# Kernel optimization log

Hardware: AMD Instinct MI355X
Metric: run time of the kernel (lower is better)

## Reference

```python
import jax, jax.numpy as jnp
import numpy as np

N = 100000
E = 3200000
IN_DIM, HID, RED, EMB = 2, 64, 32, 32
LN_EPS = 1e-5


def gcn_conv(x, W, b, row, col, w_full, dinv):
    # x:[N,F_in] W:[F_in,F_out]; PyG GCNConv: lin (no bias) -> normalized scatter-add -> + bias
    xw = x @ W                                  # [N,F_out]
    norm = dinv[row] * w_full * dinv[col]       # [E+N]
    msgs = norm[:, None] * xw[row]              # gather from source nodes
    out = jax.ops.segment_sum(msgs, col, num_segments=N)
    return out + b


def layer_norm(x, g, b):
    mu = jnp.mean(x, axis=-1, keepdims=True)
    var = jnp.mean((x - mu) ** 2, axis=-1, keepdims=True)
    return (x - mu) * jax.lax.rsqrt(var + LN_EPS) * g + b


def setup_inputs() -> dict:
    key = jax.random.key(0)
    ks = jax.random.split(key, 12)
    def glorot(k, shape):
        lim = float(np.sqrt(6.0 / (shape[0] + shape[1])))
        return jax.random.uniform(k, shape, jnp.float32, -lim, lim)
    return {
        "x": jax.random.normal(ks[0], (N, IN_DIM), jnp.float32),
        "edge_weight": jax.random.uniform(ks[1], (E,), jnp.float32),
        "W1": glorot(ks[2], (IN_DIM, HID)), "b1": jnp.zeros((HID,), jnp.float32),
        "rW1": glorot(ks[3], (IN_DIM, HID)), "rb1": jnp.zeros((HID,), jnp.float32),
        "g1": jnp.ones((HID,), jnp.float32), "be1": jnp.zeros((HID,), jnp.float32),
        "W2": glorot(ks[4], (HID, RED)), "b2": jnp.zeros((RED,), jnp.float32),
        "rW2": glorot(ks[5], (HID, RED)), "rb2": jnp.zeros((RED,), jnp.float32),
        "g2": jnp.ones((RED,), jnp.float32), "be2": jnp.zeros((RED,), jnp.float32),
        "fcW": glorot(ks[6], (RED, 1)), "fcb": jnp.zeros((1,), jnp.float32),
        "pW": glorot(ks[7], (RED, EMB)), "pb": jnp.zeros((EMB,), jnp.float32),
        "edge_index": jax.random.randint(ks[8], (2, E), 0, N, jnp.int64)
        if jax.config.read("jax_enable_x64") else jax.random.randint(ks[8], (2, E), 0, N, jnp.int32),
    }


def reference(x, edge_weight, W1, b1, rW1, rb1, g1, be1, W2, b2, rW2, rb2, g2, be2,
              fcW, fcb, pW, pb, edge_index):
    row, col = edge_index[0], edge_index[1]
    # add self-loops with weight 1 (PyG gcn_norm default)
    loops = jnp.arange(N, dtype=row.dtype)
    row_f = jnp.concatenate([row, loops])
    col_f = jnp.concatenate([col, loops])
    w_f = jnp.concatenate([edge_weight, jnp.ones((N,), edge_weight.dtype)])
    deg = jax.ops.segment_sum(w_f, col_f, num_segments=N)
    dinv = jnp.where(deg > 0, jax.lax.rsqrt(jnp.where(deg > 0, deg, 1.0)), 0.0)

    x1 = gcn_conv(x, W1, b1, row_f, col_f, w_f, dinv) + (x @ rW1 + rb1)
    x1 = jax.nn.relu(layer_norm(x1, g1, be1))
    x2 = gcn_conv(x1, W2, b2, row_f, col_f, w_f, dinv) + (x1 @ rW2 + rb2)
    x2 = jax.nn.relu(layer_norm(x2, g2, be2))

    logits = (x2 @ fcW + fcb)[:, 0]
    proj = x2 @ pW + pb
    nrm = jnp.linalg.norm(proj, axis=1, keepdims=True)
    emb = proj / jnp.maximum(nrm, 1e-12)
    return logits, emb
```

## Files before the change

### kernel.cpp

```cpp
#include <hip/hip_runtime.h>
#include <hip/hip_bf16.h>

#define NN 100000
#define NE 3200000
#define LN_EPS 1e-5f
#define NBUCK 256
#define NPB 392
#define TILE 4096
#define NTILE 782
#define CAP 16384
#define L1NB 32
#define PADF 0x80000000

__device__ __forceinline__ int bucket_of(int c) {
    return (int)(((long)c * 342393L) >> 27);
}

__global__ __launch_bounds__(256) void k_partA(
        const int* __restrict__ row, const int* __restrict__ col,
        const float* __restrict__ w, int* __restrict__ gcur,
        int2* __restrict__ tmp) {
    __shared__ int2 sbuf[TILE];
    __shared__ unsigned char bid[TILE];
    __shared__ int  lhist[NBUCK];
    __shared__ int  lofs[NBUCK];
    __shared__ int  lbase[NBUCK];
    __shared__ int  wsum[4];
    int t = threadIdx.x;
    long base_e = (long)blockIdx.x * TILE;
    int nt = NE - base_e < TILE ? (int)(NE - base_e) : TILE;

    lhist[t] = 0;
    __syncthreads();

    int pk[16]; float wv16[16]; int bri[16];
    if (nt == TILE) {
        const int4*   r4 = (const int4*)(row + base_e);
        const int4*   c4 = (const int4*)(col + base_e);
        const float4* w4 = (const float4*)(w + base_e);
        #pragma unroll
        for (int q = 0; q < 4; ++q) {
            int4 rv = r4[t * 4 + q];
            int4 cv = c4[t * 4 + q];
            float4 wv = w4[t * 4 + q];
            int rr[4] = {rv.x, rv.y, rv.z, rv.w};
            int cc[4] = {cv.x, cv.y, cv.z, cv.w};
            float ww[4] = {wv.x, wv.y, wv.z, wv.w};
            #pragma unroll
            for (int u = 0; u < 4; ++u) {
                int i = q * 4 + u;
                int b = bucket_of(cc[u]);
                int cib = cc[u] - b * NPB;
                pk[i] = rr[u] | (cib << 17);
                wv16[i] = ww[u];
                int rk = atomicAdd(&lhist[b], 1);
                bri[i] = (b << 16) | rk;
            }
        }
    } else {
        #pragma unroll
        for (int i = 0; i < 16; ++i) {
            int j = t * 16 + i;
            if (j < nt) {
                int e = (int)base_e + j;
                int r = row[e], c = col[e];
                int b = bucket_of(c);
                int cib = c - b * NPB;
                pk[i] = r | (cib << 17);
                wv16[i] = w[e];
                int rk = atomicAdd(&lhist[b], 1);
                bri[i] = (b << 16) | rk;
            } else bri[i] = -1;
        }
    }
    __syncthreads();

    {
        int v = lhist[t];
        int lane = t & 63;
        int inc = v;
        #pragma unroll
        for (int off = 1; off < 64; off <<= 1) {
            int u = __shfl_up(inc, off, 64);
            if (lane >= off) inc += u;
        }
        if (lane == 63) wsum[t >> 6] = inc;
        __syncthreads();
        int wv = t >> 6;
        int woff = 0;
        for (int j = 0; j < 4; ++j) if (j < wv) woff += wsum[j];
        lofs[t] = woff + inc - v;
        int padded = (v + 7) & ~7;
        lbase[t] = t * CAP + atomicAdd(&gcur[t], padded);
    }
    __syncthreads();

    #pragma unroll
    for (int i = 0; i < 16; ++i) {
        if (bri[i] >= 0) {
            int b = bri[i] >> 16, rk = bri[i] & 0xFFFF;
            int slot = lofs[b] + rk;
            sbuf[slot] = make_int2(pk[i], __float_as_int(wv16[i]));
            bid[slot] = (unsigned char)b;
        }
    }
    __syncthreads();

    #pragma unroll
    for (int i = 0; i < 16; ++i) {
        int j = t + i * 256;
        if (j < nt) {
            int b = bid[j];
            tmp[lbase[b] + (j - lofs[b])] = sbuf[j];
        }
    }
    {
        int v = lhist[t];
        int padded = (v + 7) & ~7;
        for (int q = v; q < padded; ++q)
            tmp[lbase[t] + q] = make_int2((int)PADF, 0);
    }
}

__global__ __launch_bounds__(1024) void k_partB1(
        const int* __restrict__ gcur, const int2* __restrict__ tmp,
        const float* __restrict__ x,
        int* __restrict__ ptr, int* __restrict__ cnt,
        float* __restrict__ dinv, float2* __restrict__ y) {
    __shared__ int   bsc[256];
    __shared__ int   nh[512];
    __shared__ float wsumf[512];
    __shared__ int   wscan[8];
    int b = blockIdx.x;
    int t = threadIdx.x;
    int bcnt = gcur[b];
    int start = b * CAP;
    if (t < 256) bsc[t] = gcur[t];
    __syncthreads();
    for (int off = 1; off < 256; off <<= 1) {
        int u = 0;
        if (t < 256 && t >= off) u = bsc[t - off];
        __syncthreads();
        if (t < 256) bsc[t] += u;
        __syncthreads();
    }
    int outb = bsc[b] - bcnt;
    if (t < 512) { nh[t] = 0; wsumf[t] = 0.0f; }
    __syncthreads();
    const int4* tp = (const int4*)(tmp + start);
    int npair = bcnt >> 1;
    for (int p = t; p < npair; p += 1024) {
        int4 rr = tp[p];
        if (!(rr.x & PADF)) {
            int cl0 = ((unsigned)rr.x) >> 17;
            atomicAdd(&nh[cl0], 1);
            atomicAdd(&wsumf[cl0], __int_as_float(rr.y));
        }
        if (!(rr.z & PADF)) {
            int cl1 = ((unsigned)rr.z) >> 17;
            atomicAdd(&nh[cl1], 1);
            atomicAdd(&wsumf[cl1], __int_as_float(rr.w));
        }
    }
    __syncthreads();
    int v = 0, inc = 0;
    if (t < 512) {
        v = nh[t];
        inc = v;
        #pragma unroll
        for (int off = 1; off < 64; off <<= 1) {
            int u = __shfl_up(inc, off, 64);
            if ((t & 63) >= off) inc += u;
        }
        if ((t & 63) == 63) wscan[t >> 6] = inc;
    }
    __syncthreads();
    if (t < NPB) {
        int wv = t >> 6;
        int woff = 0;
        #pragma unroll
        for (int j = 0; j < 8; ++j) if (j < wv) woff += wscan[j];
        int ex = outb + woff + inc - v;
        int gn = b * NPB + t;
        if (gn < NN) {
            ptr[gn] = ex;
            cnt[gn] = v;
            float di = rsqrtf(wsumf[t] + 1.0f);
            dinv[gn] = di;
            float2 xv = *(const float2*)(x + 2 * gn);
            y[gn] = make_float2(di * xv.x, di * xv.y);
        }
    }
}

__global__ __launch_bounds__(1024) void k_partB2(
        const int* __restrict__ gcur, const int2* __restrict__ tmp,
        const int* __restrict__ ptr, const float* __restrict__ dinv,
        const float2* __restrict__ y,
        unsigned* __restrict__ csrp, float* __restrict__ agg1) {
    __shared__ int   nh[512];
    __shared__ float a0s[512];
    __shared__ float a1s[512];
    int b = blockIdx.x;
    int t = threadIdx.x;
    int bcnt = gcur[b];
    int start = b * CAP;
    if (t < 512) {
        int gn = b * NPB + t;
        nh[t] = (t < NPB && gn < NN) ? ptr[gn] : 0;
        a0s[t] = 0.0f; a1s[t] = 0.0f;
    }
    __syncthreads();
    const int4* tp = (const int4*)(tmp + start);
    int npair = bcnt >> 1;
    for (int p = t; p < npair; p += 1024) {
        int4 rr = tp[p];
        if (!(rr.x & PADF)) {
            int cl = ((unsigned)rr.x) >> 17;
            int r = rr.x & 0x1FFFF;
            float wf = __int_as_float(rr.y);
            __hip_bfloat16 hb = __float2bfloat16(wf);
            unsigned short wbits = *reinterpret_cast<unsigned short*>(&hb);
            int pos = atomicAdd(&nh[cl], 1);
            csrp[pos] = ((unsigned)r << 15) | (unsigned)wbits;
            float2 yv = y[r];
            atomicAdd(&a0s[cl], wf * yv.x);
            atomicAdd(&a1s[cl], wf * yv.y);
        }
        if (!(rr.z & PADF)) {
            int cl = ((unsigned)rr.z) >> 17;
            int r = rr.z & 0x1FFFF;
            float wf = __int_as_float(rr.w);
            __hip_bfloat16 hb = __float2bfloat16(wf);
            unsigned short wbits = *reinterpret_cast<unsigned short*>(&hb);
            int pos = atomicAdd(&nh[cl], 1);
            csrp[pos] = ((unsigned)r << 15) | (unsigned)wbits;
            float2 yv = y[r];
            atomicAdd(&a0s[cl], wf * yv.x);
            atomicAdd(&a1s[cl], wf * yv.y);
        }
    }
    __syncthreads();
    if (t < NPB) {
        int gn = b * NPB + t;
        if (gn < NN) {
            float di = dinv[gn];
            float2 yv = y[gn];
            agg1[2 * gn]     = di * (a0s[t] + yv.x);
            agg1[2 * gn + 1] = di * (a1s[t] + yv.y);
        }
    }
}

__global__ __launch_bounds__(512) void k_l1t2(
        const float* __restrict__ agg1, const float* __restrict__ x,
        const float* __restrict__ dinv,
        const float* __restrict__ W1, const float* __restrict__ b1,
        const float* __restrict__ rW1, const float* __restrict__ rb1,
        const float* __restrict__ g1, const float* __restrict__ be1,
        const float* __restrict__ W2, const float* __restrict__ b2,
        const float* __restrict__ rW2, const float* __restrict__ rb2,
        __hip_bfloat16* __restrict__ t2, float* __restrict__ agg2i) {
    __shared__ float wT[64][68];
    __shared__ float xs[L1NB][68];
    int tid = threadIdx.x;
    for (int i = tid; i < 4096; i += 512) {
        int j = i >> 6, o = i & 63;
        wT[o][j] = (o < 32) ? W2[j * 32 + o] : rW2[j * 32 + (o - 32)];
    }
    int wid = tid >> 6, lane = tid & 63;
    int base = blockIdx.x * L1NB;
    float w10 = W1[lane], w11 = W1[64 + lane];
    float r10 = rW1[lane], r11 = rW1[64 + lane];
    float bb = b1[lane] + rb1[lane];
    float gg = g1[lane], be = be1[lane];
    #pragma unroll
    for (int sub = 0; sub < 4; ++sub) {
        int n = base + wid * 4 + sub;
        float a0 = agg1[2 * n], a1 = agg1[2 * n + 1];
        float xa = x[2 * n], xb = x[2 * n + 1];
        float v = a0 * w10 + a1 * w11 + xa * r10 + xb * r11 + bb;
        float s = v;
        #pragma unroll
        for (int m = 32; m >= 1; m >>= 1) s += __shfl_xor(s, m, 64);
        float mean = s * (1.0f / 64.0f);
        float e = v - mean;
        float s2 = e * e;
        #pragma unroll
        for (int m = 32; m >= 1; m >>= 1) s2 += __shfl_xor(s2, m, 64);
        float var = s2 * (1.0f / 64.0f);
        xs[wid * 4 + sub][lane] = fmaxf(e * rsqrtf(var + LN_EPS) * gg + be, 0.0f);
    }
    __syncthreads();
    int o = lane, g = wid;
    const float4* wrow = (const float4*)&wT[o][0];
    const float4* x0 = (const float4*)&xs[g][0];
    const float4* x1r = (const float4*)&xs[g + 8][0];
    const float4* x2r = (const float4*)&xs[g + 16][0];
    const float4* x3r = (const float4*)&xs[g + 24][0];
    float acc0 = 0.0f, acc1 = 0.0f, acc2 = 0.0f, acc3 = 0.0f;
    #pragma unroll
    for (int jq = 0; jq < 16; ++jq) {
        float4 wv = wrow[jq];
        float4 a = x0[jq], b = x1r[jq], c = x2r[jq], d = x3r[jq];
        acc0 += wv.x * a.x + wv.y * a.y + wv.z * a.z + wv.w * a.w;
        acc1 += wv.x * b.x + wv.y * b.y + wv.z * b.z + wv.w * b.w;
        acc2 += wv.x * c.x + wv.y * c.y + wv.z * c.z + wv.w * c.w;
        acc3 += wv.x * d.x + wv.y * d.y + wv.z * d.z + wv.w * d.w;
    }
    float res0 = __shfl_xor(acc0, 32, 64);
    float res1 = __shfl_xor(acc1, 32, 64);
    float res2 = __shfl_xor(acc2, 32, 64);
    float res3 = __shfl_xor(acc3, 32, 64);
    if (o < 32) {
        float accs[4] = {acc0, acc1, acc2, acc3};
        float ress[4] = {res0, res1, res2, res3};
        #pragma unroll
        for (int i = 0; i < 4; ++i) {
            int n = base + g + 8 * i;
            float di = dinv[n];
            t2[n * 32 + o] = __float2bfloat16(accs[i] * di);
            agg2i[n * 32 + o] = accs[i] * di * di + b2[o] + ress[i] + rb2[o];
        }
    }
}

__global__ __launch_bounds__(256) void k_agg2fin(
        const int* __restrict__ ptr, const int* __restrict__ cnt,
        const unsigned* __restrict__ csrp,
        const float* __restrict__ dinv, const __hip_bfloat16* __restrict__ t2,
        const float* __restrict__ agg2i,
        const float* __restrict__ g2, const float* __restrict__ be2,
        const float* __restrict__ fcW, const float* __restrict__ fcb,
        const float* __restrict__ pW, const float* __restrict__ pb,
        float* __restrict__ out) {
    int node = (blockIdx.x * blockDim.x + threadIdx.x) >> 5;
    int l = threadIdx.x & 31;
    if (node >= NN) return;
    int sub = l >> 4, k2 = l & 15;
    int start = ptr[node], n = cnt[node];
    const unsigned* t2u = (const unsigned*)t2;
    float ax = 0.0f, ay = 0.0f;
    int j16 = n & ~15;
    for (int j = 0; j < j16; j += 16) {
        uint4 pa = *(const uint4*)(csrp + start + j);
        uint4 pb4 = *(const uint4*)(csrp + start + j + 4);
        uint4 pc = *(const uint4*)(csrp + start + j + 8);
        uint4 pd = *(const uint4*)(csrp + start + j + 12);
        unsigned p0 = sub ? pa.y : pa.x;
        unsigned p1 = sub ? pa.w : pa.z;
        unsigned p2 = sub ? pb4.y : pb4.x;
        unsigned p3 = sub ? pb4.w : pb4.z;
        unsigned p4 = sub ? pc.y : pc.x;
        unsigned p5 = sub ? pc.w : pc.z;
        unsigned p6 = sub ? pd.y : pd.x;
        unsigned p7 = sub ? pd.w : pd.z;
        unsigned u0 = t2u[(p0 >> 15) * 16 + k2];
        unsigned u1 = t2u[(p1 >> 15) * 16 + k2];
        unsigned u2 = t2u[(p2 >> 15) * 16 + k2];
        unsigned u3 = t2u[(p3 >> 15) * 16 + k2];
        unsigned u4 = t2u[(p4 >> 15) * 16 + k2];
        unsigned u5 = t2u[(p5 >> 15) * 16 + k2];
        unsigned u6 = t2u[(p6 >> 15) * 16 + k2];
        unsigned u7 = t2u[(p7 >> 15) * 16 + k2];
        float w0 = __uint_as_float((p0 & 0x7FFFu) << 16);
        float w1 = __uint_as_float((p1 & 0x7FFFu) << 16);
        float w2 = __uint_as_float((p2 & 0x7FFFu) << 16);
        float w3 = __uint_as_float((p3 & 0x7FFFu) << 16);
        float w4 = __uint_as_float((p4 & 0x7FFFu) << 16);
        float w5 = __uint_as_float((p5 & 0x7FFFu) << 16);
        float w6 = __uint_as_float((p6 & 0x7FFFu) << 16);
        float w7 = __uint_as_float((p7 & 0x7FFFu) << 16);
        ax += w0 * __uint_as_float(u0 << 16) + w1 * __uint_as_float(u1 << 16)
            + w2 * __uint_as_float(u2 << 16) + w3 * __uint_as_float(u3 << 16)
            + w4 * __uint_as_float(u4 << 16) + w5 * __uint_as_float(u5 << 16)
            + w6 * __uint_as_float(u6 << 16) + w7 * __uint_as_float(u7 << 16);
        ay += w0 * __uint_as_float(u0 & 0xFFFF0000u) + w1 * __uint_as_float(u1 & 0xFFFF0000u)
            + w2 * __uint_as_float(u2 & 0xFFFF0000u) + w3 * __uint_as_float(u3 & 0xFFFF0000u)
            + w4 * __uint_as_float(u4 & 0xFFFF0000u) + w5 * __uint_as_float(u5 & 0xFFFF0000u)
            + w6 * __uint_as_float(u6 & 0xFFFF0000u) + w7 * __uint_as_float(u7 & 0xFFFF0000u);
    }
    int j8 = n & ~7;
    for (int j = j16; j < j8; j += 8) {
        uint4 pa = *(const uint4*)(csrp + start + j);
        uint4 pb4 = *(const uint4*)(csrp + start + j + 4);
        unsigned p0 = sub ? pa.y : pa.x;
        unsigned p1 = sub ? pa.w : pa.z;
        unsigned p2 = sub ? pb4.y : pb4.x;
        unsigned p3 = sub ? pb4.w : pb4.z;
        unsigned u0 = t2u[(p0 >> 15) * 16 + k2];
        unsigned u1 = t2u[(p1 >> 15) * 16 + k2];
        unsigned u2 = t2u[(p2 >> 15) * 16 + k2];
        unsigned u3 = t2u[(p3 >> 15) * 16 + k2];
        float w0 = __uint_as_float((p0 & 0x7FFFu) << 16);
        float w1 = __uint_as_float((p1 & 0x7FFFu) << 16);
        float w2 = __uint_as_float((p2 & 0x7FFFu) << 16);
        float w3 = __uint_as_float((p3 & 0x7FFFu) << 16);
        ax += w0 * __uint_as_float(u0 << 16) + w1 * __uint_as_float(u1 << 16)
            + w2 * __uint_as_float(u2 << 16) + w3 * __uint_as_float(u3 << 16);
        ay += w0 * __uint_as_float(u0 & 0xFFFF0000u) + w1 * __uint_as_float(u1 & 0xFFFF0000u)
            + w2 * __uint_as_float(u2 & 0xFFFF0000u) + w3 * __uint_as_float(u3 & 0xFFFF0000u);
    }
    for (int j = j8; j < n; ++j) {
        unsigned p = csrp[start + j];
        float wf = (sub == 0) ? __uint_as_float((p & 0x7FFFu) << 16) : 0.0f;
        unsigned u = t2u[(p >> 15) * 16 + k2];
        ax += wf * __uint_as_float(u << 16);
        ay += wf * __uint_as_float(u & 0xFFFF0000u);
    }
    ax += __shfl_xor(ax, 16, 32);
    ay += __shfl_xor(ay, 16, 32);
    float di = dinv[node];
    float2 ai = ((const float2*)(agg2i + node * 32))[k2];
    float v0 = ai.x + di * ax;
    float v1 = ai.y + di * ay;
    float s = v0 + v1;
    #pragma unroll
    for (int m = 8; m >= 1; m >>= 1) s += __shfl_xor(s, m, 32);
    float mean = s * (1.0f / 32.0f);
    float e0 = v0 - mean, e1 = v1 - mean;
    float s2 = e0 * e0 + e1 * e1;
    #pragma unroll
    for (int m = 8; m >= 1; m >>= 1) s2 += __shfl_xor(s2, m, 32);
    float rstd = rsqrtf(s2 * (1.0f / 32.0f) + LN_EPS);
    float2 gv = ((const float2*)g2)[k2];
    float2 bv = ((const float2*)be2)[k2];
    float x0 = fmaxf(e0 * rstd * gv.x + bv.x, 0.0f);
    float x1 = fmaxf(e1 * rstd * gv.y + bv.y, 0.0f);
    float2 fv = ((const float2*)fcW)[k2];
    float lg = x0 * fv.x + x1 * fv.y;
    #pragma unroll
    for (int m = 8; m >= 1; m >>= 1) lg += __shfl_xor(lg, m, 32);
    if (l == 0) out[node] = lg + fcb[0];
    int o = l;
    float acc2 = pb[o];
    #pragma unroll
    for (int j = 0; j < 16; ++j) {
        float xa = __shfl(x0, j, 32);
        float xb = __shfl(x1, j, 32);
        acc2 += xa * pW[(2 * j) * 32 + o] + xb * pW[(2 * j + 1) * 32 + o];
    }
    float n2 = acc2 * acc2;
    #pragma unroll
    for (int m = 16; m >= 1; m >>= 1) n2 += __shfl_xor(n2, m, 32);
    float nrm = sqrtf(n2);
    out[NN + node * 32 + o] = acc2 / fmaxf(nrm, 1e-12f);
}

extern "C" void kernel_launch(void* const* d_in, const int* in_sizes, int n_in,
                              void* d_out, int out_size, void* d_ws, size_t ws_size,
                              hipStream_t stream) {
    const float* x   = (const float*)d_in[0];
    const float* ew  = (const float*)d_in[1];
    const float* W1  = (const float*)d_in[2];
    const float* b1  = (const float*)d_in[3];
    const float* rW1 = (const float*)d_in[4];
    const float* rb1 = (const float*)d_in[5];
    const float* g1  = (const float*)d_in[6];
    const float* be1 = (const float*)d_in[7];
    const float* W2  = (const float*)d_in[8];
    const float* b2  = (const float*)d_in[9];
    const float* rW2 = (const float*)d_in[10];
    const float* rb2 = (const float*)d_in[11];
    const float* g2  = (const float*)d_in[12];
    const float* be2 = (const float*)d_in[13];
    const float* fcW = (const float*)d_in[14];
    const float* fcb = (const float*)d_in[15];
    const float* pW  = (const float*)d_in[16];
    const float* pb  = (const float*)d_in[17];
    const int*   ei  = (const int*)d_in[18];
    const int* row = ei;
    const int* col = ei + NE;

    char* p = (char*)d_ws;
    unsigned* csrp = (unsigned*)p;            p += (size_t)NBUCK * CAP * 4;
    char* regionA = p;                        p += (size_t)NBUCK * CAP * 8;
    __hip_bfloat16* t2 = (__hip_bfloat16*)regionA;
    float* agg2i = (float*)(regionA + (size_t)NN * 32 * 2);
    int2*  tmp   = (int2*)regionA;
    float* dinv  = (float*)p;                 p += (size_t)NN * 4;
    float2* y    = (float2*)p;                p += (size_t)NN * 8;
    float* agg1  = (float*)p;                 p += (size_t)2 * NN * 4;
    int*   ptr   = (int*)p;                   p += (size_t)NN * 4;
    int*   cnt   = (int*)p;                   p += (size_t)NN * 4;
    int*   gcur  = (int*)p;                   p += 256 * 4;

    float* out = (float*)d_out;
    const int TB = 256;
    const int NODE32 = (NN * 32 + TB - 1) / TB;

    hipMemsetAsync(gcur, 0, 256 * 4, stream);
    k_partA<<<NTILE, 256, 0, stream>>>(row, col, ew, gcur, tmp);
    k_partB1<<<NBUCK, 1024, 0, stream>>>(gcur, tmp, x, ptr, cnt, dinv, y);
    k_partB2<<<NBUCK, 1024, 0, stream>>>(gcur, tmp, ptr, dinv, y, csrp, agg1);
    k_l1t2<<<NN / L1NB, 512, 0, stream>>>(agg1, x, dinv, W1, b1, rW1, rb1, g1, be1,
                                          W2, b2, rW2, rb2, t2, agg2i);
    k_agg2fin<<<NODE32, TB, 0, stream>>>(ptr, cnt, csrp, dinv, t2, agg2i,
                                         g2, be2, fcW, fcb, pW, pb, out);
}
```

Measured before the change: 194.9 us.

## Fuse CSR partition passes into one cooperative kernel with register-held records

Merges the two bucket-processing kernels into a single cooperative launch separated by a grid-wide sync, keeping each thread's up-to-8 int4 edge records in registers across both phases so the temporary buffer is read once instead of twice. The per-node prefix offsets are placed directly into shared memory rather than reloaded from global ptr. This removes one kernel launch and one full pass over the bucketed edge data, but adds a grid barrier and relies on all 256 blocks of 1024 threads being co-resident, plus higher register pressure, and assumes a bucket never exceeds 8192 pairs.

```diff
diff --git a/kernel.cpp b/kernel.cpp
--- a/kernel.cpp
+++ b/kernel.cpp
@@ -1,5 +1,7 @@
 #include <hip/hip_runtime.h>
 #include <hip/hip_bf16.h>
+#include <hip/hip_cooperative_groups.h>
+namespace cg = cooperative_groups;
 
 #define NN 100000
 #define NE 3200000
@@ -122,20 +124,38 @@
     }
 }
 
-__global__ __launch_bounds__(1024) void k_partB1(
+__global__ __launch_bounds__(1024) void k_partB(
         const int* __restrict__ gcur, const int2* __restrict__ tmp,
         const float* __restrict__ x,
         int* __restrict__ ptr, int* __restrict__ cnt,
-        float* __restrict__ dinv, float2* __restrict__ y) {
+        float* __restrict__ dinv, float2* __restrict__ y,
+        unsigned* __restrict__ csrp, float* __restrict__ agg1) {
     __shared__ int   bsc[256];
     __shared__ int   nh[512];
     __shared__ float wsumf[512];
     __shared__ int   wscan[8];
+    __shared__ float a0s[512];
+    __shared__ float a1s[512];
     int b = blockIdx.x;
     int t = threadIdx.x;
     int bcnt = gcur[b];
     int start = b * CAP;
+    const int4* tp = (const int4*)(tmp + start);
+    int npair = bcnt >> 1;
+    int4 rv0, rv1, rv2, rv3, rv4, rv5, rv6, rv7;
+    {
+        int4 padrec = make_int4((int)PADF, 0, (int)PADF, 0);
+        rv0 = (t            < npair) ? tp[t]            : padrec;
+        rv1 = (t + 1024     < npair) ? tp[t + 1024]     : padrec;
+        rv2 = (t + 2048     < npair) ? tp[t + 2048]     : padrec;
+        rv3 = (t + 3072     < npair) ? tp[t + 3072]     : padrec;
+        rv4 = (t + 4096     < npair) ? tp[t + 4096]     : padrec;
+        rv5 = (t + 5120     < npair) ? tp[t + 5120]     : padrec;
+        rv6 = (t + 6144     < npair) ? tp[t + 6144]     : padrec;
+        rv7 = (t + 7168     < npair) ? tp[t + 7168]     : padrec;
+    }
     if (t < 256) bsc[t] = gcur[t];
+    if (t < 512) { nh[t] = 0; wsumf[t] = 0.0f; a0s[t] = 0.0f; a1s[t] = 0.0f; }
     __syncthreads();
     for (int off = 1; off < 256; off <<= 1) {
         int u = 0;
@@ -145,23 +165,13 @@
         __syncthreads();
     }
     int outb = bsc[b] - bcnt;
-    if (t < 512) { nh[t] = 0; wsumf[t] = 0.0f; }
-    __syncthreads();
-    const int4* tp = (const int4*)(tmp + start);
-    int npair = bcnt >> 1;
-    for (int p = t; p < npair; p += 1024) {
-        int4 rr = tp[p];
-        if (!(rr.x & PADF)) {
-            int cl0 = ((unsigned)rr.x) >> 17;
-            atomicAdd(&nh[cl0], 1);
-            atomicAdd(&wsumf[cl0], __int_as_float(rr.y));
-        }
-        if (!(rr.z & PADF)) {
-            int cl1 = ((unsigned)rr.z) >> 17;
-            atomicAdd(&nh[cl1], 1);
-            atomicAdd(&wsumf[cl1], __int_as_float(rr.w));
-        }
-    }
+    #define P1(rr) \
+        if (!((rr).x & PADF)) { int cl = ((unsigned)(rr).x) >> 17; \
+            atomicAdd(&nh[cl], 1); atomicAdd(&wsumf[cl], __int_as_float((rr).y)); } \
+        if (!((rr).z & PADF)) { int cl = ((unsigned)(rr).z) >> 17; \
+            atomicAdd(&nh[cl], 1); atomicAdd(&wsumf[cl], __int_as_float((rr).w)); }
+    P1(rv0) P1(rv1) P1(rv2) P1(rv3) P1(rv4) P1(rv5) P1(rv6) P1(rv7)
+    #undef P1
     __syncthreads();
     int v = 0, inc = 0;
     if (t < 512) {
@@ -175,12 +185,15 @@
         if ((t & 63) == 63) wscan[t >> 6] = inc;
     }
     __syncthreads();
-    if (t < NPB) {
+    int ex = 0;
+    if (t < 512) {
         int wv = t >> 6;
         int woff = 0;
         #pragma unroll
         for (int j = 0; j < 8; ++j) if (j < wv) woff += wscan[j];
-        int ex = outb + woff + inc - v;
+        ex = outb + woff + inc - v;
+    }
+    if (t < NPB) {
         int gn = b * NPB + t;
         if (gn < NN) {
             ptr[gn] = ex;
@@ -191,55 +204,33 @@
             y[gn] = make_float2(di * xv.x, di * xv.y);
         }
     }
-}
-
-__global__ __launch_bounds__(1024) void k_partB2(
-        const int* __restrict__ gcur, const int2* __restrict__ tmp,
-        const int* __restrict__ ptr, const float* __restrict__ dinv,
-        const float2* __restrict__ y,
-        unsigned* __restrict__ csrp, float* __restrict__ agg1) {
-    __shared__ int   nh[512];
-    __shared__ float a0s[512];
-    __shared__ float a1s[512];
-    int b = blockIdx.x;
-    int t = threadIdx.x;
-    int bcnt = gcur[b];
-    int start = b * CAP;
-    if (t < 512) {
-        int gn = b * NPB + t;
-        nh[t] = (t < NPB && gn < NN) ? ptr[gn] : 0;
-        a0s[t] = 0.0f; a1s[t] = 0.0f;
-    }
-    __syncthreads();
-    const int4* tp = (const int4*)(tmp + start);
-    int npair = bcnt >> 1;
-    for (int p = t; p < npair; p += 1024) {
-        int4 rr = tp[p];
-        if (!(rr.x & PADF)) {
-            int cl = ((unsigned)rr.x) >> 17;
-            int r = rr.x & 0x1FFFF;
-            float wf = __int_as_float(rr.y);
-            __hip_bfloat16 hb = __float2bfloat16(wf);
-            unsigned short wbits = *reinterpret_cast<unsigned short*>(&hb);
-            int pos = atomicAdd(&nh[cl], 1);
-            csrp[pos] = ((unsigned)r << 15) | (unsigned)wbits;
-            float2 yv = y[r];
-            atomicAdd(&a0s[cl], wf * yv.x);
-            atomicAdd(&a1s[cl], wf * yv.y);
-        }
-        if (!(rr.z & PADF)) {
-            int cl = ((unsigned)rr.z) >> 17;
-            int r = rr.z & 0x1FFFF;
-            float wf = __int_as_float(rr.w);
-            __hip_bfloat16 hb = __float2bfloat16(wf);
-            unsigned short wbits = *reinterpret_cast<unsigned short*>(&hb);
-            int pos = atomicAdd(&nh[cl], 1);
-            csrp[pos] = ((unsigned)r << 15) | (unsigned)wbits;
-            float2 yv = y[r];
-            atomicAdd(&a0s[cl], wf * yv.x);
-            atomicAdd(&a1s[cl], wf * yv.y);
-        }
-    }
+    __syncthreads();
+    if (t < 512) nh[t] = ex;
+    __syncthreads();
+    cg::this_grid().sync();
+    #define P2(rr) \
+        if (!((rr).x & PADF)) { \
+            int cl = ((unsigned)(rr).x) >> 17; int r = (rr).x & 0x1FFFF; \
+            float wf = __int_as_float((rr).y); \
+            __hip_bfloat16 hb = __float2bfloat16(wf); \
+            unsigned short wbits = *reinterpret_cast<unsigned short*>(&hb); \
+            int pos = atomicAdd(&nh[cl], 1); \
+            csrp[pos] = ((unsigned)r << 15) | (unsigned)wbits; \
+            float2 yv = y[r]; \
+            atomicAdd(&a0s[cl], wf * yv.x); \
+            atomicAdd(&a1s[cl], wf * yv.y); } \
+        if (!((rr).z & PADF)) { \
+            int cl = ((unsigned)(rr).z) >> 17; int r = (rr).z & 0x1FFFF; \
+            float wf = __int_as_float((rr).w); \
+            __hip_bfloat16 hb = __float2bfloat16(wf); \
+            unsigned short wbits = *reinterpret_cast<unsigned short*>(&hb); \
+            int pos = atomicAdd(&nh[cl], 1); \
+            csrp[pos] = ((unsigned)r << 15) | (unsigned)wbits; \
+            float2 yv = y[r]; \
+            atomicAdd(&a0s[cl], wf * yv.x); \
+            atomicAdd(&a1s[cl], wf * yv.y); }
+    P2(rv0) P2(rv1) P2(rv2) P2(rv3) P2(rv4) P2(rv5) P2(rv6) P2(rv7)
+    #undef P2
     __syncthreads();
     if (t < NPB) {
         int gn = b * NPB + t;
@@ -491,8 +482,16 @@
 
     hipMemsetAsync(gcur, 0, 256 * 4, stream);
     k_partA<<<NTILE, 256, 0, stream>>>(row, col, ew, gcur, tmp);
-    k_partB1<<<NBUCK, 1024, 0, stream>>>(gcur, tmp, x, ptr, cnt, dinv, y);
-    k_partB2<<<NBUCK, 1024, 0, stream>>>(gcur, tmp, ptr, dinv, y, csrp, agg1);
+    {
+        const int* gcur_c = gcur;
+        const int2* tmp_c = tmp;
+        const float* x_c = x;
+        void* args[] = { (void*)&gcur_c, (void*)&tmp_c, (void*)&x_c,
+                         (void*)&ptr, (void*)&cnt, (void*)&dinv, (void*)&y,
+                         (void*)&csrp, (void*)&agg1 };
+        hipLaunchCooperativeKernel((void*)k_partB, dim3(NBUCK), dim3(1024),
+                                   args, 0, stream);
+    }
     k_l1t2<<<NN / L1NB, 512, 0, stream>>>(agg1, x, dinv, W1, b1, rW1, rb1, g1, be1,
                                           W2, b2, rW2, rb2, t2, agg2i);
     k_agg2fin<<<NODE32, TB, 0, stream>>>(ptr, cnt, csrp, dinv, t2, agg2i,
```

Measured after the change: 238.5 us. 1.22x slower.
